# Kernel optimization log

Hardware: AMD Instinct MI355X
Metric: run time of the kernel (lower is better)

The kernel has to match this reference:

```python
import jax, jax.numpy as jnp
import numpy as np

B, C, H, W = 2, 256, 192, 192
STRIDE = 8


def conv2d(x, w, b, pad_h, pad_w):
    y = jax.lax.conv_general_dilated(
        x, w, window_strides=(1, 1),
        padding=[(pad_h, pad_h), (pad_w, pad_w)],
        dimension_numbers=('NCHW', 'OIHW', 'NCHW'))
    return y + b[None, :, None, None]


def rotated_feature_align(feat, boxes, spatial_scale):
    # feat: [B,C,Hf,Wf]; boxes: [B,Hf*Wf,5] per-pixel rboxes in image coords.
    # points=1: bilinearly sample feat at each pixel's box center and add to feat,
    # matching mmcv's rotated_feature_align forward kernel (incl. its (y,x) read order
    # and ROI-Align-style border handling).
    Bf, Cf, Hf, Wf = feat.shape
    y = boxes[..., 0].reshape(Bf, Hf, Wf) * spatial_scale
    x = boxes[..., 1].reshape(Bf, Hf, Wf) * spatial_scale
    valid = (y >= -1.0) & (y <= Hf) & (x >= -1.0) & (x <= Wf)
    y = jnp.maximum(y, 0.0)
    x = jnp.maximum(x, 0.0)
    yl0 = jnp.floor(y).astype(jnp.int32)
    xl0 = jnp.floor(x).astype(jnp.int32)
    ey = yl0 >= Hf - 1
    ex = xl0 >= Wf - 1
    yl = jnp.where(ey, Hf - 1, yl0)
    yh = jnp.where(ey, Hf - 1, jnp.minimum(yl0 + 1, Hf - 1))
    xl = jnp.where(ex, Wf - 1, xl0)
    xh = jnp.where(ex, Wf - 1, jnp.minimum(xl0 + 1, Wf - 1))
    y = jnp.where(ey, jnp.asarray(Hf - 1, feat.dtype), y)
    x = jnp.where(ex, jnp.asarray(Wf - 1, feat.dtype), x)
    ly = y - yl.astype(feat.dtype)
    lx = x - xl.astype(feat.dtype)
    hy = 1.0 - ly
    hx = 1.0 - lx
    ft = jnp.transpose(feat, (0, 2, 3, 1))  # [B,Hf,Wf,C]
    bi = jnp.arange(Bf)[:, None, None]
    v = ((hy * hx)[..., None] * ft[bi, yl, xl]
         + (hy * lx)[..., None] * ft[bi, yl, xh]
         + (ly * hx)[..., None] * ft[bi, yh, xl]
         + (ly * lx)[..., None] * ft[bi, yh, xh])
    v = jnp.where(valid[..., None], v, 0.0)
    return feat + jnp.transpose(v, (0, 3, 1, 2))


def setup_inputs() -> dict:
    key = jax.random.key(0)
    ks = jax.random.split(key, 9)
    x = jax.random.normal(ks[0], (B, C, H, W), dtype=jnp.float32)
    img = float(H * STRIDE)
    cy = jax.random.uniform(ks[1], (B, H * W), minval=0.0, maxval=img)
    cx = jax.random.uniform(ks[2], (B, H * W), minval=0.0, maxval=img)
    bw = jax.random.uniform(ks[3], (B, H * W), minval=8.0, maxval=64.0)
    bh = jax.random.uniform(ks[4], (B, H * W), minval=8.0, maxval=64.0)
    ba = jax.random.uniform(ks[5], (B, H * W), minval=-np.pi / 2, maxval=np.pi / 2)
    best_rbboxes = jnp.stack([cy, cx, bw, bh, ba], axis=-1)  # [B, H*W, 5]
    std = 0.01  # normal_init(std=0.01)
    w51 = jax.random.normal(ks[6], (C, C, 5, 1), dtype=jnp.float32) * std
    w15 = jax.random.normal(ks[7], (C, C, 1, 5), dtype=jnp.float32) * std
    w11 = jax.random.normal(ks[8], (C, C, 1, 1), dtype=jnp.float32) * std
    b51 = jnp.zeros((C,), jnp.float32)
    b15 = jnp.zeros((C,), jnp.float32)
    b11 = jnp.zeros((C,), jnp.float32)
    return {"x": x, "best_rbboxes": best_rbboxes, "w51": w51, "b51": b51,
            "w15": w15, "b15": b15, "w11": w11, "b11": b11}


def reference(x, best_rbboxes, w51, b51, w15, b15, w11, b11):
    # conv_5_1(conv_1_5(x)) + conv_1_1(x), then rotated feature alignment, then residual.
    feat = conv2d(conv2d(x, w15, b15, 0, 2), w51, b51, 2, 0) + conv2d(x, w11, b11, 0, 0)
    refined = rotated_feature_align(feat, best_rbboxes, 1.0 / STRIDE)
    return x + refined
```

## Files before the change

kernel.cpp:

```cpp
#include <hip/hip_runtime.h>
#include <hip/hip_bf16.h>
#include <stdint.h>

#define B_ 2
#define C_ 256
#define H_ 192
#define W_ 192
#define HW_ (H_*W_)
#define CHW_ (C_*HW_)
#define P_ (B_*HW_)
#define SCALE 0.125f

typedef __attribute__((ext_vector_type(8))) short bf16x8;
typedef __attribute__((ext_vector_type(4))) float f32x4;

__device__ __forceinline__ void gload_lds16(const void* g, void* l) {
  __builtin_amdgcn_global_load_lds(
      (const __attribute__((address_space(1))) uint32_t*)g,
      (__attribute__((address_space(3))) uint32_t*)l, 16, 0, 0);
}

__global__ __launch_bounds__(256) void wtrans_kernel(
    const float* __restrict__ w15, const float* __restrict__ w51,
    const float* __restrict__ w11,
    __hip_bfloat16* __restrict__ w1t, __hip_bfloat16* __restrict__ w2t,
    __hip_bfloat16* __restrict__ zbuf) {
  int i = blockIdx.x * 256 + threadIdx.x;
  if (i < C_ * C_ * 5) {
    int co = i / (C_ * 5);
    int r  = i - co * (C_ * 5);
    int ci = r / 5;
    int k  = r - ci * 5;
    w1t[(size_t)co * 1280 + k * 256 + ci] = __float2bfloat16(w15[i]);
    w2t[(size_t)co * 1536 + k * 256 + ci] = __float2bfloat16(w51[i]);
  }
  if (i < C_ * C_) {
    int co = i >> 8, ci = i & 255;
    w2t[(size_t)co * 1536 + 1280 + ci] = __float2bfloat16(w11[i]);
  }
  if (i < 1024) zbuf[i] = __float2bfloat16(0.f);
}

__global__ __launch_bounds__(256) void nchw2nhwc_kernel(
    const float* __restrict__ x, __hip_bfloat16* __restrict__ xT) {
  __shared__ float tile[32][33];
  int p0 = blockIdx.x * 32, c0 = blockIdx.y * 32, b = blockIdx.z;
  int tx = threadIdx.x, ty = threadIdx.y;
  const float* xb = x + (size_t)b * CHW_;
#pragma unroll
  for (int j = 0; j < 4; ++j)
    tile[ty + j * 8][tx] = xb[(size_t)(c0 + ty + j * 8) * HW_ + p0 + tx];
  __syncthreads();
  __hip_bfloat16* xo = xT + (size_t)b * HW_ * C_;
#pragma unroll
  for (int j = 0; j < 4; ++j)
    xo[(size_t)(p0 + ty + j * 8) * C_ + c0 + tx] = __float2bfloat16(tile[tx][ty + j * 8]);
}

#define AB1 25600
__global__ __launch_bounds__(256, 3) void gemm1_kernel(
    const __hip_bfloat16* __restrict__ xT, const __hip_bfloat16* __restrict__ w1t,
    const float* __restrict__ b15, __hip_bfloat16* __restrict__ t1,
    const __hip_bfloat16* __restrict__ zbuf) {
  __shared__ __align__(16) char lds[AB1 + 16384];
  int bid = blockIdx.x;
  bid = (bid & 7) * 96 + (bid >> 3);
  const int nb = bid & 1, bh = bid >> 1;
  const int p0 = bh * 192;
  const int tid = threadIdx.x, l = tid & 63, wid = tid >> 6;
  const int wrow = (wid >> 1) * 96, wcol = (wid & 1) * 64;
  const int sboff = (((l & 7) ^ (l >> 3)) << 4);
  const int lrow = l >> 3;
  const int corow0 = nb * 128;

  int b_ad[4][2];
#pragma unroll
  for (int n = 0; n < 4; ++n)
#pragma unroll
    for (int kk = 0; kk < 2; ++kk)
      b_ad[n][kk] = AB1 + (wcol + n * 16 + (l & 15)) * 128 +
                    (((kk * 4 + (l >> 4)) ^ ((l & 15) & 7)) << 4);

  f32x4 acc[6][4] = {};
  const char* xTb = (const char*)xT;
  const char* wB  = (const char*)w1t;
  const char* zb  = (const char*)zbuf;

  for (int cib = 0; cib < 4; ++cib) {
    for (int is = wid; is < 25; is += 4) {
      int row = is * 8 + lrow;
      const char* src = ((unsigned)(row - 4) < 192u)
          ? xTb + (size_t)(p0 + row - 4) * 512 + cib * 128 + sboff
          : zb + sboff;
      gload_lds16(src, lds + is * 1024);
    }
    for (int k = 0; k < 5; ++k) {
      int boff = k * 512 + cib * 128;
#pragma unroll
      for (int ii = 0; ii < 4; ++ii) {
        int is = wid * 4 + ii;
        const char* bs = wB + (size_t)(corow0 + is * 8 + lrow) * 2560 + boff + sboff;
        gload_lds16(bs, lds + AB1 + is * 1024);
      }
      __syncthreads();
      int x8 = ((l & 15) + k + 2) & 7;
      int arow0 = wrow + (l & 15) + k + 2;
#pragma unroll
      for (int kk = 0; kk < 2; ++kk) {
        int ablk = ((kk * 4 + (l >> 4)) ^ x8) << 4;
        bf16x8 bfr[4];
#pragma unroll
        for (int n = 0; n < 4; ++n) bfr[n] = *(const bf16x8*)(lds + b_ad[n][kk]);
#pragma unroll
        for (int m = 0; m < 6; ++m) {
          bf16x8 af = *(const bf16x8*)(lds + (arow0 + m * 16) * 128 + ablk);
#pragma unroll
          for (int n = 0; n < 4; ++n)
            acc[m][n] = __builtin_amdgcn_mfma_f32_16x16x32_bf16(af, bfr[n], acc[m][n], 0, 0, 0);
        }
      }
      __syncthreads();
    }
  }
#pragma unroll
  for (int n = 0; n < 4; ++n) {
    int co = corow0 + wcol + n * 16 + (l & 15);
    float bias = b15[co];
#pragma unroll
    for (int m = 0; m < 6; ++m) {
      int prow = p0 + wrow + m * 16 + (l >> 4) * 4;
#pragma unroll
      for (int r = 0; r < 4; ++r)
        t1[(size_t)(prow + r) * 256 + co] = __float2bfloat16(acc[m][n][r] + bias);
    }
  }
}

#define A2SZ 24576
#define B2OFF 49152
__global__ __launch_bounds__(512, 4) void gemm2_kernel(
    const __hip_bfloat16* __restrict__ t1, const __hip_bfloat16* __restrict__ xT,
    const __hip_bfloat16* __restrict__ w2t,
    const float* __restrict__ b51, const float* __restrict__ b11,
    __hip_bfloat16* __restrict__ featT, const __hip_bfloat16* __restrict__ zbuf) {
  __shared__ __align__(16) char lds[81920];
  int bid = blockIdx.x;
  bid = (bid & 7) * 96 + (bid >> 3);
  const int nb = bid & 1, bh = bid >> 1;
  const int p0 = bh * 192;
  const int h = bh % 192;
  const int tid = threadIdx.x, l = tid & 63, wid = tid >> 6;
  const int wrow = (wid >> 1) * 48, wcol = (wid & 1) * 64;
  const int sboff = (((l & 7) ^ (l >> 3)) << 4);
  const int lrow = l >> 3;
  const int corow0 = nb * 128;

  const char* t1b = (const char*)t1;
  const char* xTb = (const char*)xT;
  const char* wB  = (const char*)w2t;
  const char* zb  = (const char*)zbuf;

  auto stageA = [&](int s, int buf) {
    const char* abase;
    if (s < 20) {
      int k = s >> 2, cib = s & 3, dl = k - 2;
      abase = ((unsigned)(h + dl) < 192u)
          ? t1b + (size_t)(p0 + dl * 192) * 512 + cib * 128
          : (const char*)0;
    } else {
      abase = xTb + (size_t)p0 * 512 + (s - 20) * 128;
    }
#pragma unroll
    for (int i = 0; i < 3; ++i) {
      int slot = i * 8 + wid;
      int row = slot * 8 + lrow;
      const char* src = abase ? abase + (size_t)row * 512 + sboff : zb + sboff;
      gload_lds16(src, lds + buf * A2SZ + slot * 1024);
    }
  };
  auto stageB = [&](int s, int buf) {
    int boff = (s < 20) ? (s >> 2) * 512 + (s & 3) * 128 : 2560 + (s - 20) * 128;
#pragma unroll
    for (int i = 0; i < 2; ++i) {
      int slot = i * 8 + wid;
      const char* bs = wB + (size_t)(corow0 + slot * 8 + lrow) * 3072 + boff + sboff;
      gload_lds16(bs, lds + B2OFF + buf * 16384 + slot * 1024);
    }
  };

  f32x4 acc[3][4] = {};
  stageA(0, 0);
  stageB(0, 0);
  for (int t = 0; t < 24; ++t) {
    const int cur = t & 1, nxt = cur ^ 1;
    if (t < 23) {
      stageA(t + 1, nxt);
      asm volatile("s_waitcnt vmcnt(3)" ::: "memory");
    } else {
      asm volatile("s_waitcnt vmcnt(0)" ::: "memory");
    }
    __builtin_amdgcn_s_barrier();
    __builtin_amdgcn_sched_barrier(0);
    const char* la = lds + cur * A2SZ;
    const char* lb = lds + B2OFF + cur * 16384;
    {
      bf16x8 af[3], bfr[4];
#pragma unroll
      for (int m = 0; m < 3; ++m)
        af[m] = *(const bf16x8*)(la + (wrow + m * 16 + (l & 15)) * 128 +
                 (((l >> 4) ^ ((l & 15) & 7)) << 4));
#pragma unroll
      for (int n = 0; n < 4; ++n)
        bfr[n] = *(const bf16x8*)(lb + (wcol + n * 16 + (l & 15)) * 128 +
                 (((l >> 4) ^ ((l & 15) & 7)) << 4));
      __builtin_amdgcn_s_setprio(1);
#pragma unroll
      for (int m = 0; m < 3; ++m)
#pragma unroll
        for (int n = 0; n < 4; ++n)
          acc[m][n] = __builtin_amdgcn_mfma_f32_16x16x32_bf16(af[m], bfr[n], acc[m][n], 0, 0, 0);
      __builtin_amdgcn_s_setprio(0);
    }
    if (t < 23) stageB(t + 1, nxt);
    {
      bf16x8 af[3], bfr[4];
#pragma unroll
      for (int m = 0; m < 3; ++m)
        af[m] = *(const bf16x8*)(la + (wrow + m * 16 + (l & 15)) * 128 +
                 (((4 + (l >> 4)) ^ ((l & 15) & 7)) << 4));
#pragma unroll
      for (int n = 0; n < 4; ++n)
        bfr[n] = *(const bf16x8*)(lb + (wcol + n * 16 + (l & 15)) * 128 +
                 (((4 + (l >> 4)) ^ ((l & 15) & 7)) << 4));
      __builtin_amdgcn_s_setprio(1);
#pragma unroll
      for (int m = 0; m < 3; ++m)
#pragma unroll
        for (int n = 0; n < 4; ++n)
          acc[m][n] = __builtin_amdgcn_mfma_f32_16x16x32_bf16(af[m], bfr[n], acc[m][n], 0, 0, 0);
      __builtin_amdgcn_s_setprio(0);
    }
    __builtin_amdgcn_sched_barrier(0);
    __builtin_amdgcn_s_barrier();
    __builtin_amdgcn_sched_barrier(0);
  }
#pragma unroll
  for (int n = 0; n < 4; ++n) {
    int co = corow0 + wcol + n * 16 + (l & 15);
    float bias = b51[co] + b11[co];
#pragma unroll
    for (int m = 0; m < 3; ++m) {
      int prow = p0 + wrow + m * 16 + (l >> 4) * 4;
#pragma unroll
      for (int r = 0; r < 4; ++r)
        featT[(size_t)(prow + r) * 256 + co] = __float2bfloat16(acc[m][n][r] + bias);
    }
  }
}

__global__ __launch_bounds__(256) void align_kernel(
    const __hip_bfloat16* __restrict__ xT, const __hip_bfloat16* __restrict__ featT,
    const float* __restrict__ boxes, float* __restrict__ out) {
  __shared__ float vs[32][258];
  const int tid = threadIdx.x, l = tid & 63, wv = tid >> 6;
  const int p0 = blockIdx.x * 32;

#pragma unroll 4
  for (int i = 0; i < 8; ++i) {
    int pl = wv * 8 + i;
    int p = p0 + pl;
    int b = p / HW_;
    int p2 = p - b * HW_;
    float yy = boxes[(size_t)p * 5 + 0] * SCALE;
    float xx = boxes[(size_t)p * 5 + 1] * SCALE;
    bool valid = (yy >= -1.0f) && (yy <= (float)H_) && (xx >= -1.0f) && (xx <= (float)W_);
    yy = fmaxf(yy, 0.f);
    xx = fmaxf(xx, 0.f);
    int yl = (int)floorf(yy), xl = (int)floorf(xx);
    int yh, xh;
    if (yl >= H_ - 1) { yl = H_ - 1; yh = H_ - 1; yy = (float)(H_ - 1); } else { yh = yl + 1; }
    if (xl >= W_ - 1) { xl = W_ - 1; xh = W_ - 1; xx = (float)(W_ - 1); } else { xh = xl + 1; }
    float ly = yy - (float)yl, lx = xx - (float)xl;
    float hy = 1.f - ly, hx = 1.f - lx;
    float q00 = hy * hx, q01 = hy * lx, q10 = ly * hx, q11 = ly * lx;
    if (!valid) { q00 = 0.f; q01 = 0.f; q10 = 0.f; q11 = 0.f; }
    const unsigned short* fT = (const unsigned short*)featT + (size_t)b * HW_ * C_;
    const unsigned short* xb = (const unsigned short*)xT + (size_t)b * HW_ * C_;
    int co = l * 4;
    uint2 A  = *(const uint2*)(fT + ((size_t)yl * W_ + xl) * C_ + co);
    uint2 Bv = *(const uint2*)(fT + ((size_t)yl * W_ + xh) * C_ + co);
    uint2 Cv = *(const uint2*)(fT + ((size_t)yh * W_ + xl) * C_ + co);
    uint2 D  = *(const uint2*)(fT + ((size_t)yh * W_ + xh) * C_ + co);
    uint2 E  = *(const uint2*)(fT + (size_t)p2 * C_ + co);
    uint2 X  = *(const uint2*)(xb + (size_t)p2 * C_ + co);
    float o[4];
#pragma unroll
    for (int w = 0; w < 2; ++w) {
      unsigned int aw = (&A.x)[w], bw = (&Bv.x)[w], cw = (&Cv.x)[w],
                   dw = (&D.x)[w], ew = (&E.x)[w], xw = (&X.x)[w];
      float a0 = __uint_as_float(aw << 16), a1 = __uint_as_float(aw & 0xffff0000u);
      float b0 = __uint_as_float(bw << 16), b1 = __uint_as_float(bw & 0xffff0000u);
      float c0 = __uint_as_float(cw << 16), c1 = __uint_as_float(cw & 0xffff0000u);
      float d0 = __uint_as_float(dw << 16), d1 = __uint_as_float(dw & 0xffff0000u);
      float e0 = __uint_as_float(ew << 16), e1 = __uint_as_float(ew & 0xffff0000u);
      float x0 = __uint_as_float(xw << 16), x1 = __uint_as_float(xw & 0xffff0000u);
      o[w * 2 + 0] = x0 + e0 + q00 * a0 + q01 * b0 + q10 * c0 + q11 * d0;
      o[w * 2 + 1] = x1 + e1 + q00 * a1 + q01 * b1 + q10 * c1 + q11 * d1;
    }
    *(float2*)&vs[pl][co]     = make_float2(o[0], o[1]);
    *(float2*)&vs[pl][co + 2] = make_float2(o[2], o[3]);
  }
  __syncthreads();

  const int pl = tid & 31, cg = tid >> 5;
  const int p = p0 + pl;
  const int b = p / HW_;
  const int p2 = p - b * HW_;
  float* oc = out + (size_t)b * CHW_ + p2;
#pragma unroll
  for (int j = 0; j < 32; ++j) {
    int ch = cg * 32 + j;
    __builtin_nontemporal_store(vs[pl][ch], &oc[(size_t)ch * HW_]);
  }
}

extern "C" void kernel_launch(void* const* d_in, const int* in_sizes, int n_in,
                              void* d_out, int out_size, void* d_ws, size_t ws_size,
                              hipStream_t stream) {
  const float* x     = (const float*)d_in[0];
  const float* boxes = (const float*)d_in[1];
  const float* w51   = (const float*)d_in[2];
  const float* b51   = (const float*)d_in[3];
  const float* w15   = (const float*)d_in[4];
  const float* b15   = (const float*)d_in[5];
  const float* w11   = (const float*)d_in[6];
  const float* b11   = (const float*)d_in[7];
  float* out = (float*)d_out;

  __hip_bfloat16* featT = (__hip_bfloat16*)d_ws;
  __hip_bfloat16* xT   = featT + (size_t)P_ * C_;
  __hip_bfloat16* w1t  = xT + (size_t)P_ * C_;
  __hip_bfloat16* w2t  = w1t + (size_t)C_ * 1280;
  __hip_bfloat16* zbuf = w2t + (size_t)C_ * 1536;
  __hip_bfloat16* t1 = (__hip_bfloat16*)d_out;

  wtrans_kernel<<<dim3((C_ * C_ * 5 + 255) / 256), 256, 0, stream>>>(
      w15, w51, w11, w1t, w2t, zbuf);
  nchw2nhwc_kernel<<<dim3(HW_ / 32, C_ / 32, B_), dim3(32, 8), 0, stream>>>(x, xT);
  gemm1_kernel<<<dim3(768), 256, 0, stream>>>(xT, w1t, b15, t1, zbuf);
  gemm2_kernel<<<dim3(768), 512, 0, stream>>>(t1, xT, w2t, b51, b11, featT, zbuf);
  align_kernel<<<dim3(P_ / 32), 256, 0, stream>>>(xT, featT, boxes, out);
}
```

Baseline: 172.6 us.

## Switch gemm2 to 32x32x16 MFMA with 4 waves and larger per-wave tiles

Rewrites the second GEMM kernel to use 32x32x16 bf16 MFMA instructions instead of 16x16x32. Each block now has 4 waves instead of 8, and each wave computes a 96x64 tile instead of 48x64. LDS read addresses are precomputed, and the staging loops are widened so each thread issues more async loads. The aim is fewer LDS fragment reads per FLOP and higher MFMA efficiency, at the cost of more accumulator registers per thread and fewer waves to hide latency.

```diff
diff --git a/kernel.cpp b/kernel.cpp
--- a/kernel.cpp
+++ b/kernel.cpp
@@ -13,6 +13,7 @@
 
 typedef __attribute__((ext_vector_type(8))) short bf16x8;
 typedef __attribute__((ext_vector_type(4))) float f32x4;
+typedef __attribute__((ext_vector_type(16))) float f32x16;
 
 __device__ __forceinline__ void gload_lds16(const void* g, void* l) {
   __builtin_amdgcn_global_load_lds(
@@ -138,7 +139,7 @@
 
 #define A2SZ 24576
 #define B2OFF 49152
-__global__ __launch_bounds__(512, 4) void gemm2_kernel(
+__global__ __launch_bounds__(256, 2) void gemm2_kernel(
     const __hip_bfloat16* __restrict__ t1, const __hip_bfloat16* __restrict__ xT,
     const __hip_bfloat16* __restrict__ w2t,
     const float* __restrict__ b51, const float* __restrict__ b11,
@@ -150,7 +151,7 @@
   const int p0 = bh * 192;
   const int h = bh % 192;
   const int tid = threadIdx.x, l = tid & 63, wid = tid >> 6;
-  const int wrow = (wid >> 1) * 48, wcol = (wid & 1) * 64;
+  const int wrow = (wid >> 1) * 96, wcol = (wid & 1) * 64;
   const int sboff = (((l & 7) ^ (l >> 3)) << 4);
   const int lrow = l >> 3;
   const int corow0 = nb * 128;
@@ -171,8 +172,8 @@
       abase = xTb + (size_t)p0 * 512 + (s - 20) * 128;
     }
 #pragma unroll
-    for (int i = 0; i < 3; ++i) {
-      int slot = i * 8 + wid;
+    for (int i = 0; i < 6; ++i) {
+      int slot = i * 4 + wid;
       int row = slot * 8 + lrow;
       const char* src = abase ? abase + (size_t)row * 512 + sboff : zb + sboff;
       gload_lds16(src, lds + buf * A2SZ + slot * 1024);
@@ -181,63 +182,70 @@
   auto stageB = [&](int s, int buf) {
     int boff = (s < 20) ? (s >> 2) * 512 + (s & 3) * 128 : 2560 + (s - 20) * 128;
 #pragma unroll
-    for (int i = 0; i < 2; ++i) {
-      int slot = i * 8 + wid;
+    for (int i = 0; i < 4; ++i) {
+      int slot = i * 4 + wid;
       const char* bs = wB + (size_t)(corow0 + slot * 8 + lrow) * 3072 + boff + sboff;
       gload_lds16(bs, lds + B2OFF + buf * 16384 + slot * 1024);
     }
   };
 
-  f32x4 acc[3][4] = {};
+  int a_ad[3][4], b_ad[2][4];
+#pragma unroll
+  for (int m = 0; m < 3; ++m)
+#pragma unroll
+    for (int k2 = 0; k2 < 4; ++k2)
+      a_ad[m][k2] = (wrow + m * 32 + (l & 31)) * 128 +
+                    (((k2 * 2 + (l >> 5)) ^ (l & 7)) << 4);
+#pragma unroll
+  for (int n = 0; n < 2; ++n)
+#pragma unroll
+    for (int k2 = 0; k2 < 4; ++k2)
+      b_ad[n][k2] = B2OFF + (wcol + n * 32 + (l & 31)) * 128 +
+                    (((k2 * 2 + (l >> 5)) ^ (l & 7)) << 4);
+
+  f32x16 acc[3][2] = {};
   stageA(0, 0);
   stageB(0, 0);
   for (int t = 0; t < 24; ++t) {
     const int cur = t & 1, nxt = cur ^ 1;
     if (t < 23) {
       stageA(t + 1, nxt);
-      asm volatile("s_waitcnt vmcnt(3)" ::: "memory");
+      asm volatile("s_waitcnt vmcnt(6)" ::: "memory");
     } else {
       asm volatile("s_waitcnt vmcnt(0)" ::: "memory");
     }
     __builtin_amdgcn_s_barrier();
     __builtin_amdgcn_sched_barrier(0);
-    const char* la = lds + cur * A2SZ;
-    const char* lb = lds + B2OFF + cur * 16384;
-    {
-      bf16x8 af[3], bfr[4];
+    const int ab = cur * A2SZ, bb = cur * 16384;
+#pragma unroll
+    for (int k2 = 0; k2 < 2; ++k2) {
+      bf16x8 af[3], bfr[2];
+#pragma unroll
+      for (int m = 0; m < 3; ++m) af[m] = *(const bf16x8*)(lds + ab + a_ad[m][k2]);
+#pragma unroll
+      for (int n = 0; n < 2; ++n) bfr[n] = *(const bf16x8*)(lds + bb + b_ad[n][k2]);
+      __builtin_amdgcn_s_setprio(1);
 #pragma unroll
       for (int m = 0; m < 3; ++m)
-        af[m] = *(const bf16x8*)(la + (wrow + m * 16 + (l & 15)) * 128 +
-                 (((l >> 4) ^ ((l & 15) & 7)) << 4));
-#pragma unroll
-      for (int n = 0; n < 4; ++n)
-        bfr[n] = *(const bf16x8*)(lb + (wcol + n * 16 + (l & 15)) * 128 +
-                 (((l >> 4) ^ ((l & 15) & 7)) << 4));
+#pragma unroll
+        for (int n = 0; n < 2; ++n)
+          acc[m][n] = __builtin_amdgcn_mfma_f32_32x32x16_bf16(af[m], bfr[n], acc[m][n], 0, 0, 0);
+      __builtin_amdgcn_s_setprio(0);
+    }
+    if (t < 23) stageB(t + 1, nxt);
+#pragma unroll
+    for (int k2 = 2; k2 < 4; ++k2) {
+      bf16x8 af[3], bfr[2];
+#pragma unroll
+      for (int m = 0; m < 3; ++m) af[m] = *(const bf16x8*)(lds + ab + a_ad[m][k2]);
+#pragma unroll
+      for (int n = 0; n < 2; ++n) bfr[n] = *(const bf16x8*)(lds + bb + b_ad[n][k2]);
       __builtin_amdgcn_s_setprio(1);
 #pragma unroll
       for (int m = 0; m < 3; ++m)
 #pragma unroll
-        for (int n = 0; n < 4; ++n)
-          acc[m][n] = __builtin_amdgcn_mfma_f32_16x16x32_bf16(af[m], bfr[n], acc[m][n], 0, 0, 0);
-      __builtin_amdgcn_s_setprio(0);
-    }
-    if (t < 23) stageB(t + 1, nxt);
-    {
-      bf16x8 af[3], bfr[4];
-#pragma unroll
-      for (int m = 0; m < 3; ++m)
-        af[m] = *(const bf16x8*)(la + (wrow + m * 16 + (l & 15)) * 128 +
-                 (((4 + (l >> 4)) ^ ((l & 15) & 7)) << 4));
-#pragma unroll
-      for (int n = 0; n < 4; ++n)
-        bfr[n] = *(const bf16x8*)(lb + (wcol + n * 16 + (l & 15)) * 128 +
-                 (((4 + (l >> 4)) ^ ((l & 15) & 7)) << 4));
-      __builtin_amdgcn_s_setprio(1);
-#pragma unroll
-      for (int m = 0; m < 3; ++m)
-#pragma unroll
-        for (int n = 0; n < 4; ++n)
-          acc[m][n] = __builtin_amdgcn_mfma_f32_16x16x32_bf16(af[m], bfr[n], acc[m][n], 0, 0, 0);
+        for (int n = 0; n < 2; ++n)
+          acc[m][n] = __builtin_amdgcn_mfma_f32_32x32x16_bf16(af[m], bfr[n], acc[m][n], 0, 0, 0);
       __builtin_amdgcn_s_setprio(0);
     }
     __builtin_amdgcn_sched_barrier(0);
@@ -245,15 +253,17 @@
     __builtin_amdgcn_sched_barrier(0);
   }
 #pragma unroll
-  for (int n = 0; n < 4; ++n) {
-    int co = corow0 + wcol + n * 16 + (l & 15);
+  for (int n = 0; n < 2; ++n) {
+    int co = corow0 + wcol + n * 32 + (l & 31);
     float bias = b51[co] + b11[co];
 #pragma unroll
     for (int m = 0; m < 3; ++m) {
-      int prow = p0 + wrow + m * 16 + (l >> 4) * 4;
-#pragma unroll
-      for (int r = 0; r < 4; ++r)
-        featT[(size_t)(prow + r) * 256 + co] = __float2bfloat16(acc[m][n][r] + bias);
+      int prow0 = p0 + wrow + m * 32 + 4 * (l >> 5);
+#pragma unroll
+      for (int r = 0; r < 16; ++r) {
+        int prow = prow0 + (r & 3) + 8 * (r >> 2);
+        featT[(size_t)prow * 256 + co] = __float2bfloat16(acc[m][n][r] + bias);
+      }
     }
   }
 }
@@ -348,6 +358,6 @@
       w15, w51, w11, w1t, w2t, zbuf);
   nchw2nhwc_kernel<<<dim3(HW_ / 32, C_ / 32, B_), dim3(32, 8), 0, stream>>>(x, xT);
   gemm1_kernel<<<dim3(768), 256, 0, stream>>>(xT, w1t, b15, t1, zbuf);
-  gemm2_kernel<<<dim3(768), 512, 0, stream>>>(t1, xT, w2t, b51, b11, featT, zbuf);
+  gemm2_kernel<<<dim3(768), 256, 0, stream>>>(t1, xT, w2t, b51, b11, featT, zbuf);
   align_kernel<<<dim3(P_ / 32), 256, 0, stream>>>(xT, featT, boxes, out);
 }
```

Result: slower. 182.1 us (+5.5%).
